# Kernel tuning notes

Measured on AMD Instinct MI355X. Metric: run time of the kernel, lower is better.

The kernel has to match this reference:

```python
import jax, jax.numpy as jnp
import numpy as np

K = 8                    # batch_k: images per class
MARGIN = 0.2
NU = 0.0
CUTOFF = 0.5
NONZERO_LOSS_CUTOFF = 1.4
EPS = 1e-8


def setup_inputs() -> dict:
    key = jax.random.key(0)
    k1, k2 = jax.random.split(key)
    n, d = 8192, 128
    x = jax.random.normal(k1, (n, d), dtype=jnp.float32)
    # unit-norm embeddings (paper assumption; keeps distances < 2 so
    # log(1 - 0.25*d^2) in the sampling weights stays finite)
    x = x / jnp.linalg.norm(x, axis=1, keepdims=True)
    y = jax.random.randint(k2, (n,), 0, 1024, dtype=jnp.int64)
    beta_in = jnp.ones((n,), dtype=jnp.float32)
    return {"x": x, "y": y, "beta_in": beta_in}


def _sampling(x, key):
    """Distance-weighted sampling. Returns (a_index, p_index, n_index),
    each of length n*(K-1). Mirrors the numpy/CPU sampling loop."""
    x = jax.lax.stop_gradient(x)        # torch code samples on detached features
    n, d = x.shape
    sq = jnp.sum(x * x, axis=1, keepdims=True)            # [n,1]
    dist2 = sq + sq.T - 2.0 * (x @ x.T)                    # [n,n]
    dist = jnp.sqrt(dist2 + jnp.eye(n, dtype=x.dtype))     # diag -> 1, as in original
    dist = jnp.maximum(dist, CUTOFF)
    # log q(d) ~ (2-d)*log(dist) - (d-3)/2 * log(1 - dist^2/4)
    log_w = (2.0 - d) * jnp.log(dist) - (d - 3) / 2.0 * jnp.log(1.0 - 0.25 * dist * dist)
    w = jnp.exp(log_w - jnp.max(log_w))
    block = jnp.arange(n) // K
    mask = (block[:, None] != block[None, :]) & (dist < NONZERO_LOSS_CUTOFF)
    w = w * mask
    row_ok = jnp.sum(w, axis=1) > 0.0
    # categorical logits: log of weights (row-normalization is irrelevant to
    # categorical sampling); fallback to uniform for degenerate rows, matching
    # the original's try/except np.random.choice fallback.
    logits = jnp.where(w > 0.0, jnp.log(w + 1e-30), -jnp.inf)
    logits = jnp.where(row_ok[:, None], logits, 0.0)
    n_index = jax.random.categorical(key, logits, shape=(K - 1, n)).T.reshape(-1)  # [n*(K-1)]

    # anchors: each i repeated K-1 times; positives: the other K-1 members of
    # i's block, in block order (self pushed last by stable argsort on bool)
    idx = jnp.arange(n)
    a_index = jnp.repeat(idx, K - 1)
    cand = (idx // K * K)[:, None] + jnp.arange(K)[None, :]        # [n,K]
    order = jnp.argsort(cand == idx[:, None], axis=1, stable=True)
    p_index = jnp.take_along_axis(cand, order, axis=1)[:, : K - 1].reshape(-1)
    return a_index, p_index, n_index


def reference(x, y, beta_in):
    a_index, p_index, n_index = _sampling(x, jax.random.key(42))
    beta_work = beta_in[a_index]
    beta_reg_loss = jnp.sum(beta_work) * NU
    anchors = x[a_index]
    positives = x[p_index]
    negatives = x[n_index]
    d_ap = jnp.sqrt(jnp.sum((anchors - positives) ** 2, axis=1) + EPS)
    d_an = jnp.sqrt(jnp.sum((anchors - negatives) ** 2, axis=1) + EPS)
    pos_loss = jax.nn.relu(d_ap - beta_work + MARGIN)
    neg_loss = jax.nn.relu(beta_work - d_an + MARGIN)
    pair_cnt = jnp.sum((pos_loss > 0.0).astype(jnp.float32) + (neg_loss > 0.0).astype(jnp.float32))
    loss = (jnp.sum(pos_loss + neg_loss) + beta_reg_loss) / pair_cnt
    return loss
```

## Files before the change

kernel.cpp:

```cpp
#include <hip/hip_runtime.h>
#include <math.h>


#define NROWS 8192
#define DDIM  128
#define NPAIRF 7.0f
#define BT 128
#define NTILE (NROWS / BT)
#define NPAIRS (NTILE * (NTILE + 1) / 2)
#define LW2_SHIFT 57.70780163555852f

typedef short bf16x8 __attribute__((ext_vector_type(8)));
typedef float f32x4  __attribute__((ext_vector_type(4)));

template <bool B> struct BoolK { static constexpr bool value = B; };

__device__ __forceinline__ unsigned short f2bf(float f) {
    unsigned int u = __float_as_uint(f);
    return (unsigned short)((u + 0x7fffu + ((u >> 16) & 1u)) >> 16);
}

__global__ void prep_kernel(const float* __restrict__ x, unsigned short* __restrict__ xb,
                            float* __restrict__ rowacc, float* __restrict__ accum) {
    int t = blockIdx.x * 256 + threadIdx.x;
    if (t < NROWS * 3) rowacc[t] = 0.0f;
    if (t < 3) accum[t] = 0.0f;
    int idx = t * 4;
    float4 v = *(const float4*)&x[idx];
    ushort4 h;
    h.x = f2bf(v.x); h.y = f2bf(v.y); h.z = f2bf(v.z); h.w = f2bf(v.w);
    *(ushort4*)&xb[idx] = h;
}

__global__ __launch_bounds__(256, 2) void gram_kernel(
        const unsigned short* __restrict__ xb,
        const float* __restrict__ beta, float* __restrict__ rowacc) {
    __shared__ unsigned short Abuf[BT * DDIM];
    __shared__ unsigned short Bbuf[BT * DDIM];

    int rem = blockIdx.x, I = 0;
    while (rem >= NTILE - I) { rem -= NTILE - I; ++I; }
    const int J = I + rem;
    const int row0 = I * BT, col0 = J * BT;

    const int tid = threadIdx.x;
    const int lane = tid & 63;
    const int wave = tid >> 6;
    const int wy = wave >> 1, wx = wave & 1;
    const int l15 = lane & 15, quad = lane >> 4;

    {
        uint4* dA = (uint4*)Abuf;
        uint4* dB = (uint4*)Bbuf;
#pragma unroll
        for (int t = 0; t < 8; t++) {
            int s = tid + t * 256;
            int row = s >> 4;
            int kb = s & 15;
            int phys = row * 16 + (kb ^ (row & 7));
            dA[phys] = *(const uint4*)&xb[(size_t)(row0 + row) * DDIM + kb * 8];
            dB[phys] = *(const uint4*)&xb[(size_t)(col0 + row) * DDIM + kb * 8];
        }
    }

    f32x4 acc[4][4];
#pragma unroll
    for (int i = 0; i < 4; i++)
#pragma unroll
        for (int j = 0; j < 4; j++) acc[i][j] = (f32x4){0.f, 0.f, 0.f, 0.f};

    __syncthreads();

#pragma unroll
    for (int kc = 0; kc < 4; kc++) {
        bf16x8 af[4], bfr[4];
#pragma unroll
        for (int i = 0; i < 4; i++) {
            int ra = wy * 64 + i * 16 + l15;
            int pa = (kc * 4 + quad) ^ (ra & 7);
            af[i] = *(const bf16x8*)&Abuf[(ra * 16 + pa) * 8];
            int rb = wx * 64 + i * 16 + l15;
            int pb = (kc * 4 + quad) ^ (rb & 7);
            bfr[i] = *(const bf16x8*)&Bbuf[(rb * 16 + pb) * 8];
        }
#pragma unroll
        for (int i = 0; i < 4; i++)
#pragma unroll
            for (int j = 0; j < 4; j++)
                acc[i][j] = __builtin_amdgcn_mfma_f32_16x16x32_bf16(
                    af[i], bfr[j], acc[i][j], 0, 0, 0);
    }

    float bpc4[4];
    int cloc4[4];
#pragma unroll
    for (int j = 0; j < 4; j++) {
        int cl = wx * 64 + j * 16 + l15;
        bpc4[j] = beta[col0 + cl] + 0.2f;
        cloc4[j] = cl >> 3;
    }
    float bpm16[16];
    int rloc16[16];
#pragma unroll
    for (int i = 0; i < 4; i++)
#pragma unroll
        for (int reg = 0; reg < 4; reg++) {
            int idx = i * 4 + reg;
            int rl = wy * 64 + i * 16 + quad * 4 + reg;
            bpm16[idx] = beta[row0 + rl] + 0.2f;
            rloc16[idx] = rl >> 3;
        }

    float ts0[16], ts1[16], ts2[16];
    float tc0[4], tc1[4], tc2[4];
#pragma unroll
    for (int k = 0; k < 16; k++) ts0[k] = ts1[k] = ts2[k] = 0.0f;
#pragma unroll
    for (int k = 0; k < 4; k++) tc0[k] = tc1[k] = tc2[k] = 0.0f;

    auto fold = [&](auto diag_c) {
        constexpr bool DIAG = decltype(diag_c)::value;
#pragma unroll
        for (int i = 0; i < 4; i++)
#pragma unroll
            for (int reg = 0; reg < 4; reg++) {
                const int idx = i * 4 + reg;
                const float bpm = bpm16[idx];
#pragma unroll
                for (int j = 0; j < 4; j++) {
                    float g = acc[i][j][reg];
                    float dist2 = fmaxf(fmaf(-2.0f, g, 2.0f), 0.0f);
                    float d = __builtin_amdgcn_sqrtf(dist2 + 1e-8f);
                    float t = fmaxf(dist2, 0.25f);
                    float u = fmaf(-0.25f, t, 1.0f);
                    float lw2 = fmaf(-63.0f, __builtin_amdgcn_logf(t),
                                fmaf(-62.5f, __builtin_amdgcn_logf(u), -LW2_SHIFT));
                    bool valid = t < 1.96f;
                    if (DIAG) valid = valid && (rloc16[idx] != cloc4[j]);
                    float w = valid ? __builtin_amdgcn_exp2f(lw2) : 0.0f;
                    float nlr = fmaxf(bpm - d, 0.0f);
                    ts0[idx] += w;
                    ts1[idx] = fmaf(w, nlr, ts1[idx]);
                    ts2[idx] += (nlr > 0.0f) ? w : 0.0f;
                    if (!DIAG) {
                        float nlc = fmaxf(bpc4[j] - d, 0.0f);
                        tc0[j] += w;
                        tc1[j] = fmaf(w, nlc, tc1[j]);
                        tc2[j] += (nlc > 0.0f) ? w : 0.0f;
                    }
                }
            }
    };
    if (I == J) fold(BoolK<true>{}); else fold(BoolK<false>{});

    float r0 = 0.f, r1 = 0.f, r2 = 0.f;
#pragma unroll
    for (int idx = 0; idx < 16; idx++) {
        float t0 = ts0[idx], t1 = ts1[idx], t2 = ts2[idx];
#pragma unroll
        for (int off = 1; off < 16; off <<= 1) {
            t0 += __shfl_xor(t0, off);
            t1 += __shfl_xor(t1, off);
            t2 += __shfl_xor(t2, off);
        }
        if (l15 == idx) { r0 = t0; r1 = t1; r2 = t2; }
    }
    {
        int rg = row0 + wy * 64 + (l15 >> 2) * 16 + quad * 4 + (l15 & 3);
        atomicAdd(&rowacc[rg * 3 + 0], r0);
        atomicAdd(&rowacc[rg * 3 + 1], r1);
        atomicAdd(&rowacc[rg * 3 + 2], r2);
    }

    if (I != J) {
        float c0 = 0.f, c1 = 0.f, c2 = 0.f;
#pragma unroll
        for (int j = 0; j < 4; j++) {
            float t0 = tc0[j], t1 = tc1[j], t2 = tc2[j];
            t0 += __shfl_xor(t0, 16); t1 += __shfl_xor(t1, 16); t2 += __shfl_xor(t2, 16);
            t0 += __shfl_xor(t0, 32); t1 += __shfl_xor(t1, 32); t2 += __shfl_xor(t2, 32);
            if (quad == j) { c0 = t0; c1 = t1; c2 = t2; }
        }
        int cg = col0 + wx * 64 + quad * 16 + l15;
        atomicAdd(&rowacc[cg * 3 + 0], c0);
        atomicAdd(&rowacc[cg * 3 + 1], c1);
        atomicAdd(&rowacc[cg * 3 + 2], c2);
    }
}

__global__ __launch_bounds__(256) void final_kernel(
        const float* __restrict__ x, const float* __restrict__ beta,
        const float* __restrict__ rowacc, float* __restrict__ accum,
        float* __restrict__ out) {
    int t = blockIdx.x * 256 + threadIdx.x;
    int i = t >> 3;
    int p = t & 7;
    int j = (i & ~7) + p;
    float betai = beta[i];
    const float4* xi = (const float4*)&x[(size_t)i * DDIM];
    const float4* xj = (const float4*)&x[(size_t)j * DDIM];
    float d2 = 0.0f;
#pragma unroll
    for (int k = 0; k < DDIM / 4; k++) {
        float4 va = xi[k], vb = xj[k];
        float dx = va.x - vb.x, dy = va.y - vb.y;
        float dz = va.z - vb.z, dw = va.w - vb.w;
        d2 = fmaf(dx, dx, fmaf(dy, dy, fmaf(dz, dz, fmaf(dw, dw, d2))));
    }
    float d = __builtin_amdgcn_sqrtf(d2 + 1e-8f);
    float nl = fmaxf(betai - d + 0.2f, 0.0f);
    float fb1 = nl;
    float fb2 = (nl > 0.0f) ? 1.0f : 0.0f;
    float num = 0.f, cnt = 0.f;
    if (j != i) {
        float pl = fmaxf(d - betai + 0.2f, 0.0f);
        num = pl;
        cnt = (pl > 0.0f) ? 1.0f : 0.0f;
    }
#pragma unroll
    for (int off = 1; off < 8; off <<= 1) {
        num += __shfl_xor(num, off); cnt += __shfl_xor(cnt, off);
        fb1 += __shfl_xor(fb1, off); fb2 += __shfl_xor(fb2, off);
    }
    if (p == 0) {
        float a0 = rowacc[i * 3 + 0], a1 = rowacc[i * 3 + 1], a2 = rowacc[i * 3 + 2];
        if (a0 > 0.0f) {
            num += NPAIRF * a1 / a0;
            cnt += NPAIRF * a2 / a0;
        } else {
            num += NPAIRF * fb1 / (float)NROWS;
            cnt += NPAIRF * fb2 / (float)NROWS;
        }
    } else {
        num = 0.f; cnt = 0.f;
    }
#pragma unroll
    for (int off = 8; off < 64; off <<= 1) {
        num += __shfl_xor(num, off);
        cnt += __shfl_xor(cnt, off);
    }
    __shared__ float sm[8];
    int wv = threadIdx.x >> 6, ln = threadIdx.x & 63;
    if (ln == 0) { sm[wv] = num; sm[4 + wv] = cnt; }
    __syncthreads();
    if (threadIdx.x == 0) {
        float n2 = 0.f, c2 = 0.f;
#pragma unroll
        for (int w = 0; w < 4; w++) { n2 += sm[w]; c2 += sm[4 + w]; }
        atomicAdd(&accum[0], n2);
        atomicAdd(&accum[1], c2);
        __threadfence();
        unsigned int old = __float_as_uint(atomicAdd(&accum[2], 1.0f));
        if (old == __float_as_uint((float)(gridDim.x - 1))) {
            float nn = atomicAdd(&accum[0], 0.0f);
            float cc = atomicAdd(&accum[1], 0.0f);
            out[0] = nn / cc;
        }
    }
}

extern "C" void kernel_launch(void* const* d_in, const int* in_sizes, int n_in,
                              void* d_out, int out_size, void* d_ws, size_t ws_size,
                              hipStream_t stream) {
    const float* x = (const float*)d_in[0];
    const float* beta = (const float*)d_in[2];
    float* out = (float*)d_out;
    float* ws = (float*)d_ws;

    float* accum = ws;
    float* rowacc = ws + 64;
    unsigned short* xb = (unsigned short*)(rowacc + NROWS * 3);

    prep_kernel<<<NROWS * DDIM / 1024, 256, 0, stream>>>(x, xb, rowacc, accum);
    gram_kernel<<<NPAIRS, 256, 0, stream>>>(xb, beta, rowacc);
    final_kernel<<<NROWS * 8 / 256, 256, 0, stream>>>(x, beta, rowacc, accum, out);
}
```

Measured before the change: 151.7 us.

## Fuse prep, gram and final into one persistent cooperative kernel

Replaces three kernel launches with a single cooperative kernel of 512 persistent blocks that run prep, then a dynamically scheduled loop over gram tile pairs (atomic work counter), then the final reduction, separated by grid-wide syncs. This removes launch gaps and the tail imbalance of the triangular tile grid. The cost is two grid barriers, an atomic fetch per tile, and a limit of 512 resident blocks. It falls back to the old three-kernel path if the cooperative launch fails.

```diff
diff --git a/kernel.cpp b/kernel.cpp
--- a/kernel.cpp
+++ b/kernel.cpp
@@ -1,5 +1,8 @@
 #include <hip/hip_runtime.h>
+#include <hip/hip_cooperative_groups.h>
 #include <math.h>
+
+namespace cg = cooperative_groups;
 
 
 #define NROWS 8192
@@ -9,6 +12,8 @@
 #define NTILE (NROWS / BT)
 #define NPAIRS (NTILE * (NTILE + 1) / 2)
 #define LW2_SHIFT 57.70780163555852f
+#define GBLK 512
+#define FINAL_BLOCKS 256
 
 typedef short bf16x8 __attribute__((ext_vector_type(8)));
 typedef float f32x4  __attribute__((ext_vector_type(4)));
@@ -20,11 +25,11 @@
     return (unsigned short)((u + 0x7fffu + ((u >> 16) & 1u)) >> 16);
 }
 
-__global__ void prep_kernel(const float* __restrict__ x, unsigned short* __restrict__ xb,
-                            float* __restrict__ rowacc, float* __restrict__ accum) {
-    int t = blockIdx.x * 256 + threadIdx.x;
+__device__ __forceinline__ void prep_body(int t, const float* __restrict__ x,
+        unsigned short* __restrict__ xb, float* __restrict__ rowacc,
+        float* __restrict__ accum) {
     if (t < NROWS * 3) rowacc[t] = 0.0f;
-    if (t < 3) accum[t] = 0.0f;
+    if (t < 8) accum[t] = 0.0f;
     int idx = t * 4;
     float4 v = *(const float4*)&x[idx];
     ushort4 h;
@@ -32,13 +37,11 @@
     *(ushort4*)&xb[idx] = h;
 }
 
-__global__ __launch_bounds__(256, 2) void gram_kernel(
-        const unsigned short* __restrict__ xb,
-        const float* __restrict__ beta, float* __restrict__ rowacc) {
-    __shared__ unsigned short Abuf[BT * DDIM];
-    __shared__ unsigned short Bbuf[BT * DDIM];
-
-    int rem = blockIdx.x, I = 0;
+__device__ __forceinline__ void gram_pair(
+        int p, const unsigned short* __restrict__ xb,
+        const float* __restrict__ beta, float* __restrict__ rowacc,
+        unsigned short* Abuf, unsigned short* Bbuf) {
+    int rem = p, I = 0;
     while (rem >= NTILE - I) { rem -= NTILE - I; ++I; }
     const int J = I + rem;
     const int row0 = I * BT, col0 = J * BT;
@@ -188,11 +191,12 @@
     }
 }
 
-__global__ __launch_bounds__(256) void final_kernel(
+__device__ __forceinline__ void final_body(
+        int bid, int tid, int nticket,
         const float* __restrict__ x, const float* __restrict__ beta,
         const float* __restrict__ rowacc, float* __restrict__ accum,
-        float* __restrict__ out) {
-    int t = blockIdx.x * 256 + threadIdx.x;
+        float* __restrict__ out, float* sm) {
+    int t = bid * 256 + tid;
     int i = t >> 3;
     int p = t & 7;
     int j = (i & ~7) + p;
@@ -239,24 +243,76 @@
         num += __shfl_xor(num, off);
         cnt += __shfl_xor(cnt, off);
     }
-    __shared__ float sm[8];
-    int wv = threadIdx.x >> 6, ln = threadIdx.x & 63;
+    int wv = tid >> 6, ln = tid & 63;
     if (ln == 0) { sm[wv] = num; sm[4 + wv] = cnt; }
     __syncthreads();
-    if (threadIdx.x == 0) {
+    if (tid == 0) {
         float n2 = 0.f, c2 = 0.f;
 #pragma unroll
         for (int w = 0; w < 4; w++) { n2 += sm[w]; c2 += sm[4 + w]; }
         atomicAdd(&accum[0], n2);
         atomicAdd(&accum[1], c2);
         __threadfence();
-        unsigned int old = __float_as_uint(atomicAdd(&accum[2], 1.0f));
-        if (old == __float_as_uint((float)(gridDim.x - 1))) {
+        float old = atomicAdd(&accum[2], 1.0f);
+        if (old == (float)(nticket - 1)) {
             float nn = atomicAdd(&accum[0], 0.0f);
             float cc = atomicAdd(&accum[1], 0.0f);
             out[0] = nn / cc;
         }
     }
+}
+
+__global__ __launch_bounds__(256, 2) void fused_kernel(
+        const float* __restrict__ x, const float* __restrict__ beta,
+        unsigned short* __restrict__ xb, float* __restrict__ rowacc,
+        float* __restrict__ accum, float* __restrict__ out) {
+    __shared__ unsigned short Abuf[BT * DDIM];
+    __shared__ unsigned short Bbuf[BT * DDIM];
+    __shared__ unsigned int s_pair;
+    cg::grid_group grid = cg::this_grid();
+    const int tid = threadIdx.x;
+    const int bid = blockIdx.x;
+
+    int t0 = bid * 256 + tid;
+    prep_body(t0, x, xb, rowacc, accum);
+    prep_body(t0 + GBLK * 256, x, xb, rowacc, accum);
+    grid.sync();
+
+    unsigned int* ctr = (unsigned int*)(accum + 3);
+    for (;;) {
+        if (tid == 0) s_pair = atomicAdd(ctr, 1u);
+        __syncthreads();
+        unsigned int p = s_pair;
+        if (p >= (unsigned int)NPAIRS) break;
+        gram_pair((int)p, xb, beta, rowacc, Abuf, Bbuf);
+    }
+    grid.sync();
+
+    if (bid < FINAL_BLOCKS) {
+        final_body(bid, tid, FINAL_BLOCKS, x, beta, rowacc, accum, out,
+                   (float*)Abuf);
+    }
+}
+
+__global__ void prep_kernel(const float* __restrict__ x, unsigned short* __restrict__ xb,
+                            float* __restrict__ rowacc, float* __restrict__ accum) {
+    prep_body(blockIdx.x * 256 + threadIdx.x, x, xb, rowacc, accum);
+}
+
+__global__ __launch_bounds__(256, 2) void gram_kernel(
+        const unsigned short* __restrict__ xb,
+        const float* __restrict__ beta, float* __restrict__ rowacc) {
+    __shared__ unsigned short Abuf[BT * DDIM];
+    __shared__ unsigned short Bbuf[BT * DDIM];
+    gram_pair(blockIdx.x, xb, beta, rowacc, Abuf, Bbuf);
+}
+
+__global__ __launch_bounds__(256) void final_kernel(
+        const float* __restrict__ x, const float* __restrict__ beta,
+        const float* __restrict__ rowacc, float* __restrict__ accum,
+        float* __restrict__ out) {
+    __shared__ float sm[8];
+    final_body(blockIdx.x, threadIdx.x, gridDim.x, x, beta, rowacc, accum, out, sm);
 }
 
 extern "C" void kernel_launch(void* const* d_in, const int* in_sizes, int n_in,
@@ -271,7 +327,14 @@
     float* rowacc = ws + 64;
     unsigned short* xb = (unsigned short*)(rowacc + NROWS * 3);
 
-    prep_kernel<<<NROWS * DDIM / 1024, 256, 0, stream>>>(x, xb, rowacc, accum);
-    gram_kernel<<<NPAIRS, 256, 0, stream>>>(xb, beta, rowacc);
-    final_kernel<<<NROWS * 8 / 256, 256, 0, stream>>>(x, beta, rowacc, accum, out);
-}
+    void* args[] = {(void*)&x, (void*)&beta, (void*)&xb,
+                    (void*)&rowacc, (void*)&accum, (void*)&out};
+    hipError_t e = hipLaunchCooperativeKernel((const void*)fused_kernel,
+                                              dim3(GBLK), dim3(256),
+                                              args, 0, stream);
+    if (e != hipSuccess) {
+        prep_kernel<<<NROWS * DDIM / 1024, 256, 0, stream>>>(x, xb, rowacc, accum);
+        gram_kernel<<<NPAIRS, 256, 0, stream>>>(xb, beta, rowacc);
+        final_kernel<<<NROWS * 8 / 256, 256, 0, stream>>>(x, beta, rowacc, accum, out);
+    }
+}
```

Measured after the change: 282.1 us. 86.0% more time.

## Fuse bf16 conversion into gram staging and replace atomics with deterministic partials

Applied to the files above, without the earlier changes.

Removes the separate prep kernel by converting fp32 to bf16 directly while staging tiles into LDS inside the gram kernel. Per-row and per-column sums are first combined across waves in shared memory, then written as per-tile partials to a workspace buffer instead of being atomically added. The final kernel sums the 64 tile partials per row and uses a last-block reduction over per-block partials. This removes one launch and the global atomic contention, at the cost of twice the fp32 global reads in staging and a larger partial buffer to write and read back.

```diff
diff --git a/kernel.cpp b/kernel.cpp
--- a/kernel.cpp
+++ b/kernel.cpp
@@ -9,6 +9,7 @@
 #define NTILE (NROWS / BT)
 #define NPAIRS (NTILE * (NTILE + 1) / 2)
 #define LW2_SHIFT 57.70780163555852f
+#define FINAL_BLOCKS 256
 
 typedef short bf16x8 __attribute__((ext_vector_type(8)));
 typedef float f32x4  __attribute__((ext_vector_type(4)));
@@ -20,23 +21,41 @@
     return (unsigned short)((u + 0x7fffu + ((u >> 16) & 1u)) >> 16);
 }
 
-__global__ void prep_kernel(const float* __restrict__ x, unsigned short* __restrict__ xb,
-                            float* __restrict__ rowacc, float* __restrict__ accum) {
+__device__ __forceinline__ void stage_from_x(const float* __restrict__ x,
+        int base_row, unsigned short* buf, int tid) {
+#pragma unroll
+    for (int t = 0; t < 8; t++) {
+        int s = tid + t * 256;
+        int row = s >> 4;
+        int kb = s & 15;
+        int phys = row * 16 + (kb ^ (row & 7));
+        const float4* src = (const float4*)&x[(size_t)(base_row + row) * DDIM + kb * 8];
+        float4 v0 = src[0], v1 = src[1];
+        uint4 pk;
+        pk.x = (unsigned)f2bf(v0.x) | ((unsigned)f2bf(v0.y) << 16);
+        pk.y = (unsigned)f2bf(v0.z) | ((unsigned)f2bf(v0.w) << 16);
+        pk.z = (unsigned)f2bf(v1.x) | ((unsigned)f2bf(v1.y) << 16);
+        pk.w = (unsigned)f2bf(v1.z) | ((unsigned)f2bf(v1.w) << 16);
+        ((uint4*)buf)[phys] = pk;
+    }
+}
+
+__global__ void prep_kernel(float* __restrict__ rowacc, float* __restrict__ accum) {
     int t = blockIdx.x * 256 + threadIdx.x;
     if (t < NROWS * 3) rowacc[t] = 0.0f;
-    if (t < 3) accum[t] = 0.0f;
-    int idx = t * 4;
-    float4 v = *(const float4*)&x[idx];
-    ushort4 h;
-    h.x = f2bf(v.x); h.y = f2bf(v.y); h.z = f2bf(v.z); h.w = f2bf(v.w);
-    *(ushort4*)&xb[idx] = h;
-}
-
+    if (t < 8) accum[t] = 0.0f;
+}
+
+template <bool DET>
 __global__ __launch_bounds__(256, 2) void gram_kernel(
-        const unsigned short* __restrict__ xb,
-        const float* __restrict__ beta, float* __restrict__ rowacc) {
+        const float* __restrict__ x, const float* __restrict__ beta,
+        float* __restrict__ Pout, float* __restrict__ accum) {
     __shared__ unsigned short Abuf[BT * DDIM];
     __shared__ unsigned short Bbuf[BT * DDIM];
+    __shared__ float comb_rows[BT][3];
+    __shared__ float comb_cols[BT][3];
+
+    if (DET && blockIdx.x == 0 && threadIdx.x == 0) accum[2] = 0.0f;
 
     int rem = blockIdx.x, I = 0;
     while (rem >= NTILE - I) { rem -= NTILE - I; ++I; }
@@ -49,19 +68,8 @@
     const int wy = wave >> 1, wx = wave & 1;
     const int l15 = lane & 15, quad = lane >> 4;
 
-    {
-        uint4* dA = (uint4*)Abuf;
-        uint4* dB = (uint4*)Bbuf;
-#pragma unroll
-        for (int t = 0; t < 8; t++) {
-            int s = tid + t * 256;
-            int row = s >> 4;
-            int kb = s & 15;
-            int phys = row * 16 + (kb ^ (row & 7));
-            dA[phys] = *(const uint4*)&xb[(size_t)(row0 + row) * DDIM + kb * 8];
-            dB[phys] = *(const uint4*)&xb[(size_t)(col0 + row) * DDIM + kb * 8];
-        }
-    }
+    stage_from_x(x, row0, Abuf, tid);
+    stage_from_x(x, col0, Bbuf, tid);
 
     f32x4 acc[4][4];
 #pragma unroll
@@ -165,34 +173,66 @@
         }
         if (l15 == idx) { r0 = t0; r1 = t1; r2 = t2; }
     }
-    {
-        int rg = row0 + wy * 64 + (l15 >> 2) * 16 + quad * 4 + (l15 & 3);
-        atomicAdd(&rowacc[rg * 3 + 0], r0);
-        atomicAdd(&rowacc[rg * 3 + 1], r1);
-        atomicAdd(&rowacc[rg * 3 + 2], r2);
-    }
-
-    if (I != J) {
-        float c0 = 0.f, c1 = 0.f, c2 = 0.f;
-#pragma unroll
-        for (int j = 0; j < 4; j++) {
-            float t0 = tc0[j], t1 = tc1[j], t2 = tc2[j];
-            t0 += __shfl_xor(t0, 16); t1 += __shfl_xor(t1, 16); t2 += __shfl_xor(t2, 16);
-            t0 += __shfl_xor(t0, 32); t1 += __shfl_xor(t1, 32); t2 += __shfl_xor(t2, 32);
-            if (quad == j) { c0 = t0; c1 = t1; c2 = t2; }
-        }
-        int cg = col0 + wx * 64 + quad * 16 + l15;
-        atomicAdd(&rowacc[cg * 3 + 0], c0);
-        atomicAdd(&rowacc[cg * 3 + 1], c1);
-        atomicAdd(&rowacc[cg * 3 + 2], c2);
-    }
-}
-
+    const int rowl = wy * 64 + (l15 >> 2) * 16 + quad * 4 + (l15 & 3);
+
+    float c0 = 0.f, c1 = 0.f, c2 = 0.f;
+#pragma unroll
+    for (int j = 0; j < 4; j++) {
+        float t0 = tc0[j], t1 = tc1[j], t2 = tc2[j];
+        t0 += __shfl_xor(t0, 16); t1 += __shfl_xor(t1, 16); t2 += __shfl_xor(t2, 16);
+        t0 += __shfl_xor(t0, 32); t1 += __shfl_xor(t1, 32); t2 += __shfl_xor(t2, 32);
+        if (quad == j) { c0 = t0; c1 = t1; c2 = t2; }
+    }
+    const int coll = wx * 64 + quad * 16 + l15;
+
+    if (wx == 0) {
+        comb_rows[rowl][0] = r0; comb_rows[rowl][1] = r1; comb_rows[rowl][2] = r2;
+    }
+    if (wy == 0 && I != J) {
+        comb_cols[coll][0] = c0; comb_cols[coll][1] = c1; comb_cols[coll][2] = c2;
+    }
+    __syncthreads();
+    if (wx == 1) {
+        float v0 = r0 + comb_rows[rowl][0];
+        float v1 = r1 + comb_rows[rowl][1];
+        float v2 = r2 + comb_rows[rowl][2];
+        int rg = row0 + rowl;
+        if (DET) {
+            Pout[(0 * NTILE + J) * NROWS + rg] = v0;
+            Pout[(1 * NTILE + J) * NROWS + rg] = v1;
+            Pout[(2 * NTILE + J) * NROWS + rg] = v2;
+        } else {
+            atomicAdd(&Pout[rg * 3 + 0], v0);
+            atomicAdd(&Pout[rg * 3 + 1], v1);
+            atomicAdd(&Pout[rg * 3 + 2], v2);
+        }
+    }
+    if (wy == 1 && I != J) {
+        float v0 = c0 + comb_cols[coll][0];
+        float v1 = c1 + comb_cols[coll][1];
+        float v2 = c2 + comb_cols[coll][2];
+        int cg = col0 + coll;
+        if (DET) {
+            Pout[(0 * NTILE + I) * NROWS + cg] = v0;
+            Pout[(1 * NTILE + I) * NROWS + cg] = v1;
+            Pout[(2 * NTILE + I) * NROWS + cg] = v2;
+        } else {
+            atomicAdd(&Pout[cg * 3 + 0], v0);
+            atomicAdd(&Pout[cg * 3 + 1], v1);
+            atomicAdd(&Pout[cg * 3 + 2], v2);
+        }
+    }
+}
+
+template <bool DET>
 __global__ __launch_bounds__(256) void final_kernel(
         const float* __restrict__ x, const float* __restrict__ beta,
-        const float* __restrict__ rowacc, float* __restrict__ accum,
-        float* __restrict__ out) {
-    int t = blockIdx.x * 256 + threadIdx.x;
+        const float* __restrict__ Pin, float* __restrict__ accum,
+        float* __restrict__ blkpart, float* __restrict__ out) {
+    __shared__ float sm[8];
+    __shared__ bool amLast;
+    const int tid = threadIdx.x;
+    int t = blockIdx.x * 256 + tid;
     int i = t >> 3;
     int p = t & 7;
     int j = (i & ~7) + p;
@@ -217,13 +257,25 @@
         num = pl;
         cnt = (pl > 0.0f) ? 1.0f : 0.0f;
     }
+    float a0 = 0.f, a1 = 0.f, a2 = 0.f;
+    if (DET) {
+#pragma unroll
+        for (int k = 0; k < 8; k++) {
+            int s = p + k * 8;
+            a0 += Pin[(0 * NTILE + s) * NROWS + i];
+            a1 += Pin[(1 * NTILE + s) * NROWS + i];
+            a2 += Pin[(2 * NTILE + s) * NROWS + i];
+        }
+    }
 #pragma unroll
     for (int off = 1; off < 8; off <<= 1) {
         num += __shfl_xor(num, off); cnt += __shfl_xor(cnt, off);
         fb1 += __shfl_xor(fb1, off); fb2 += __shfl_xor(fb2, off);
+        a0 += __shfl_xor(a0, off);  a1 += __shfl_xor(a1, off);
+        a2 += __shfl_xor(a2, off);
     }
     if (p == 0) {
-        float a0 = rowacc[i * 3 + 0], a1 = rowacc[i * 3 + 1], a2 = rowacc[i * 3 + 2];
+        if (!DET) { a0 = Pin[i * 3 + 0]; a1 = Pin[i * 3 + 1]; a2 = Pin[i * 3 + 2]; }
         if (a0 > 0.0f) {
             num += NPAIRF * a1 / a0;
             cnt += NPAIRF * a2 / a0;
@@ -239,22 +291,36 @@
         num += __shfl_xor(num, off);
         cnt += __shfl_xor(cnt, off);
     }
-    __shared__ float sm[8];
-    int wv = threadIdx.x >> 6, ln = threadIdx.x & 63;
+    int wv = tid >> 6, ln = tid & 63;
     if (ln == 0) { sm[wv] = num; sm[4 + wv] = cnt; }
     __syncthreads();
-    if (threadIdx.x == 0) {
+    if (tid == 0) {
         float n2 = 0.f, c2 = 0.f;
 #pragma unroll
         for (int w = 0; w < 4; w++) { n2 += sm[w]; c2 += sm[4 + w]; }
-        atomicAdd(&accum[0], n2);
-        atomicAdd(&accum[1], c2);
+        blkpart[blockIdx.x * 2 + 0] = n2;
+        blkpart[blockIdx.x * 2 + 1] = c2;
         __threadfence();
-        unsigned int old = __float_as_uint(atomicAdd(&accum[2], 1.0f));
-        if (old == __float_as_uint((float)(gridDim.x - 1))) {
-            float nn = atomicAdd(&accum[0], 0.0f);
-            float cc = atomicAdd(&accum[1], 0.0f);
+        amLast = (atomicAdd(&accum[2], 1.0f) == (float)(gridDim.x - 1));
+    }
+    __syncthreads();
+    if (amLast) {
+        __threadfence();
+        float n = blkpart[tid * 2 + 0];
+        float c = blkpart[tid * 2 + 1];
+#pragma unroll
+        for (int off = 1; off < 64; off <<= 1) {
+            n += __shfl_xor(n, off);
+            c += __shfl_xor(c, off);
+        }
+        if (ln == 0) { sm[wv] = n; sm[4 + wv] = c; }
+        __syncthreads();
+        if (tid == 0) {
+            float nn = 0.f, cc = 0.f;
+#pragma unroll
+            for (int w = 0; w < 4; w++) { nn += sm[w]; cc += sm[4 + w]; }
             out[0] = nn / cc;
+            accum[2] = 0.0f;
         }
     }
 }
@@ -268,10 +334,20 @@
     float* ws = (float*)d_ws;
 
     float* accum = ws;
-    float* rowacc = ws + 64;
-    unsigned short* xb = (unsigned short*)(rowacc + NROWS * 3);
-
-    prep_kernel<<<NROWS * DDIM / 1024, 256, 0, stream>>>(x, xb, rowacc, accum);
-    gram_kernel<<<NPAIRS, 256, 0, stream>>>(xb, beta, rowacc);
-    final_kernel<<<NROWS * 8 / 256, 256, 0, stream>>>(x, beta, rowacc, accum, out);
-}
+    float* blkpart = ws + 64;
+    float* P = blkpart + FINAL_BLOCKS * 2;
+
+    const size_t det_bytes = (64 + FINAL_BLOCKS * 2
+                              + (size_t)3 * NTILE * NROWS) * 4;
+    if (ws_size >= det_bytes) {
+        gram_kernel<true><<<NPAIRS, 256, 0, stream>>>(x, beta, P, accum);
+        final_kernel<true><<<FINAL_BLOCKS, 256, 0, stream>>>(x, beta, P, accum,
+                                                             blkpart, out);
+    } else {
+        float* rowacc = blkpart + FINAL_BLOCKS * 2;
+        prep_kernel<<<(NROWS * 3 + 255) / 256, 256, 0, stream>>>(rowacc, accum);
+        gram_kernel<false><<<NPAIRS, 256, 0, stream>>>(x, beta, rowacc, accum);
+        final_kernel<false><<<FINAL_BLOCKS, 256, 0, stream>>>(x, beta, rowacc, accum,
+                                                              blkpart, out);
+    }
+}
```

Result: faster. 131.5 us (-13.3%).
